# Kernel optimization log

Hardware: AMD Instinct MI355X
Metric: run time of the kernel (lower is better)

The kernel has to match this reference:

```python
import jax, jax.numpy as jnp
import numpy as np

ARCH = [128, 64, 32]
HIDDEN = 256
N_NODES = 20000
N_EDGES = 640000


def setup_inputs() -> dict:
    key = jax.random.key(0)
    ks = jax.random.split(key, 10)
    s = lambda fan_in: 1.0 / np.sqrt(fan_in)
    inp = {
        "x": jax.random.normal(ks[0], (N_NODES, ARCH[0]), dtype=jnp.float32),
        "edge_index": jax.random.randint(ks[1], (2, N_EDGES), 0, N_NODES, dtype=jnp.int64),
        # embedding: Linear(arch[0], hidden)
        "emb_W": jax.random.uniform(ks[2], (HIDDEN, ARCH[0]), jnp.float32, -s(ARCH[0]), s(ARCH[0])),
        "emb_b": jax.random.uniform(ks[3], (HIDDEN,), jnp.float32, -s(ARCH[0]), s(ARCH[0])),
        # message: Linear(hidden, hidden)
        "msg_W": jax.random.uniform(ks[4], (HIDDEN, HIDDEN), jnp.float32, -s(HIDDEN), s(HIDDEN)),
        "msg_b": jax.random.uniform(ks[5], (HIDDEN,), jnp.float32, -s(HIDDEN), s(HIDDEN)),
        # output_layers[0]: Linear(hidden, arch[0]*arch[1]) = 256 -> 8192
        "W0": jax.random.uniform(ks[6], (ARCH[0] * ARCH[1], HIDDEN), jnp.float32, -s(HIDDEN), s(HIDDEN)),
        "b0": jax.random.uniform(ks[7], (ARCH[0] * ARCH[1],), jnp.float32, -s(HIDDEN), s(HIDDEN)),
        # output_layers[1]: Linear(hidden, arch[1]*arch[2]) = 256 -> 2048
        "W1": jax.random.uniform(ks[8], (ARCH[1] * ARCH[2], HIDDEN), jnp.float32, -s(HIDDEN), s(HIDDEN)),
        "b1": jax.random.uniform(ks[9], (ARCH[1] * ARCH[2],), jnp.float32, -s(HIDDEN), s(HIDDEN)),
    }
    return inp


def reference(x, edge_index, emb_W, emb_b, msg_W, msg_b, W0, b0, W1, b1):
    # h = relu(embedding(x)): [N, hidden]
    h = jax.nn.relu(x @ emb_W.T + emb_b)
    row, col = edge_index[0], edge_index[1]
    # gather messages from source nodes, scatter-add into destinations
    agg = jnp.zeros_like(h).at[row].add(h[col])  # [N, hidden]
    h = jax.nn.relu(agg @ msg_W.T + msg_b)       # [N, hidden]
    # per-layer weight prediction: linear, reshape, mean over nodes
    w0 = (h @ W0.T + b0).mean(axis=0).reshape(ARCH[0], ARCH[1])  # [128, 64]
    w1 = (h @ W1.T + b1).mean(axis=0).reshape(ARCH[1], ARCH[2])  # [64, 32]
    return (w0, w1)
```

## Files before the change

### kernel.cpp

```cpp
#include <hip/hip_runtime.h>
#include <hip/hip_bf16.h>

#define N_NODES 20000
#define N_EDGES 640000
#define HID 256
#define INDIM 128

#define WS_H_OFF    0u
#define WS_AGG_OFF  5120000u
#define WS_EW_OFF   15360000u
#define WS_MW_OFF   15425536u
#define WS_CS_OFF   15556608u
#define WS_DEG_OFF  15557632u
#define WS_ROW_OFF  15637632u
#define WS_SRC_OFF  15717760u
#define WS_NEEDED   18277760u

#define EW_ELEMS (HID * INDIM)
#define MW_ELEMS (HID * HID)
#define CONV_BLOCKS ((EW_ELEMS + MW_ELEMS) / 8 / 256)
#define ZERO_BYTES  (1024 + 80000)
#define ZERO_F4     (ZERO_BYTES / 16)
#define ZERO_BLOCKS ((ZERO_F4 + 255) / 256)

#define EMB_BLOCKS  ((N_NODES + 63) / 64)
#define CNT_BLOCKS  (N_EDGES / 256)

typedef __attribute__((ext_vector_type(8))) short bf16x8;
typedef __attribute__((ext_vector_type(4))) float f32x4;
typedef __attribute__((ext_vector_type(2))) float f32x2;

__device__ inline unsigned short f2bf(float v) {
    union { float f; unsigned int u; } c; c.f = v;
    unsigned int lsb = (c.u >> 16) & 1u;
    c.u += 0x7fffu + lsb;
    return (unsigned short)(c.u >> 16);
}

__device__ inline unsigned char f2fp8(float v) {
    union { float f; unsigned int u; } c; c.f = v;
    if (v == 0.f) return 0;
    int e = (int)((c.u >> 23) & 0xff) - 127;
    if (e >= -6) {
        unsigned int mant = c.u & 0x7fffffu;
        unsigned int base = ((unsigned int)(e + 7) << 3) | (mant >> 20);
        unsigned int rem  = mant & 0xfffffu;
        base += (rem > 0x80000u) || (rem == 0x80000u && (base & 1u));
        return (unsigned char)base;
    } else {
        return (unsigned char)__builtin_rintf(v * 512.0f);
    }
}

__global__ __launch_bounds__(256) void k_convert(const float* __restrict__ eW,
                                                 const float* __restrict__ mW,
                                                 unsigned short* __restrict__ eWbf,
                                                 unsigned short* __restrict__ mWbf,
                                                 float4* __restrict__ zbase)
{
    if (blockIdx.x >= CONV_BLOCKS) {
        const int zi = (blockIdx.x - CONV_BLOCKS) * 256 + threadIdx.x;
        if (zi < ZERO_F4) zbase[zi] = make_float4(0.f, 0.f, 0.f, 0.f);
        return;
    }
    const int t = blockIdx.x * 256 + threadIdx.x;
    const int i8 = t * 8;
    const float* src;
    unsigned short* dst;
    int off;
    if (i8 < EW_ELEMS) { src = eW; dst = eWbf; off = i8; }
    else               { src = mW; dst = mWbf; off = i8 - EW_ELEMS; }

    float4 a = *(const float4*)(src + off);
    float4 b = *(const float4*)(src + off + 4);
    unsigned short o[8] = { f2bf(a.x), f2bf(a.y), f2bf(a.z), f2bf(a.w),
                            f2bf(b.x), f2bf(b.y), f2bf(b.z), f2bf(b.w) };
    *(bf16x8*)(dst + off) = *(bf16x8*)o;
}

__global__ __launch_bounds__(256) void k_embed_count(const float* __restrict__ x,
                                                     const unsigned short* __restrict__ Wbf,
                                                     const float* __restrict__ b,
                                                     unsigned char* __restrict__ h8,
                                                     const int* __restrict__ ei,
                                                     int* __restrict__ deg)
{
    if (blockIdx.x >= EMB_BLOCKS) {
        const int e = (blockIdx.x - EMB_BLOCKS) * 256 + threadIdx.x;
        if (e < N_EDGES) atomicAdd(&deg[ei[e]], 1);
        return;
    }

    const int tid  = threadIdx.x;
    const int wave = tid >> 6;
    const int lane = tid & 63;
    const int lr   = lane & 15;
    const int lq   = lane >> 4;
    const int n0   = blockIdx.x * 64;
    const int colbase = wave * 64;

    f32x4 acc[4][4] = {};

#pragma unroll
    for (int kk = 0; kk < INDIM; kk += 32) {
        bf16x8 a[4], bb[4];
#pragma unroll
        for (int g = 0; g < 4; ++g) {
            const float* xr = x + (size_t)(n0 + g * 16 + lr) * INDIM + kk + lq * 8;
            uint4 p0 = *(const uint4*)xr;
            uint4 p1 = *(const uint4*)(xr + 4);
            union { unsigned u[4]; bf16x8 v; } pk;
            pk.u[0] = ((p0.x + 0x8000u) >> 16) | ((p0.y + 0x8000u) & 0xFFFF0000u);
            pk.u[1] = ((p0.z + 0x8000u) >> 16) | ((p0.w + 0x8000u) & 0xFFFF0000u);
            pk.u[2] = ((p1.x + 0x8000u) >> 16) | ((p1.y + 0x8000u) & 0xFFFF0000u);
            pk.u[3] = ((p1.z + 0x8000u) >> 16) | ((p1.w + 0x8000u) & 0xFFFF0000u);
            a[g] = pk.v;
        }
#pragma unroll
        for (int c = 0; c < 4; ++c)
            bb[c] = *(const bf16x8*)(Wbf + (size_t)(colbase + c * 16 + lr) * INDIM + kk + lq * 8);
#pragma unroll
        for (int g = 0; g < 4; ++g)
#pragma unroll
            for (int c = 0; c < 4; ++c)
                acc[g][c] = __builtin_amdgcn_mfma_f32_16x16x32_bf16(a[g], bb[c], acc[g][c], 0, 0, 0);
    }

#pragma unroll
    for (int c = 0; c < 4; ++c) {
        const int j = colbase + c * 16 + lr;
        const float bias = b[j];
#pragma unroll
        for (int g = 0; g < 4; ++g) {
            const int nbase = n0 + g * 16 + lq * 4;
#pragma unroll
            for (int r = 0; r < 4; ++r) {
                const int n = nbase + r;
                if (n < N_NODES) {
                    float v = acc[g][c][r] + bias;
                    v = v > 0.f ? v : 0.f;
                    h8[(size_t)n * HID + j] = f2fp8(v);
                }
            }
        }
    }
}

__global__ __launch_bounds__(1024) void k_scan(const int* __restrict__ deg,
                                               int* __restrict__ rowstart)
{
    __shared__ int sums[1024];
    const int t = threadIdx.x;
    const int per = 20;
    const int base = t * per;

    int local[per];
    int s = 0;
#pragma unroll
    for (int i = 0; i < per; ++i) {
        int idx = base + i;
        int v = (idx < N_NODES) ? deg[idx] : 0;
        local[i] = s;
        s += v;
    }
    sums[t] = s;
    __syncthreads();

    for (int off = 1; off < 1024; off <<= 1) {
        int v = 0;
        if (t >= off) v = sums[t - off];
        __syncthreads();
        if (t >= off) sums[t] += v;
        __syncthreads();
    }

    const int pre = (t == 0) ? 0 : sums[t - 1];
#pragma unroll
    for (int i = 0; i < per; ++i) {
        int idx = base + i;
        if (idx < N_NODES) rowstart[idx] = pre + local[i];
    }
    if (t == 1023) rowstart[N_NODES] = sums[1023];
}

__global__ __launch_bounds__(256) void k_fill(const int* __restrict__ ei,
                                              const int* __restrict__ rowstart,
                                              int* __restrict__ deg,
                                              int* __restrict__ srcs)
{
    const int e = blockIdx.x * 256 + threadIdx.x;
    if (e >= N_EDGES) return;
    const int dst = ei[e];
    const int src = ei[N_EDGES + e];
    const int pos = rowstart[dst] + atomicSub(&deg[dst], 1) - 1;
    srcs[pos] = src;
}

__global__ __launch_bounds__(256) void k_gather(const int* __restrict__ rowstart,
                                                const int* __restrict__ srcs,
                                                const unsigned char* __restrict__ h8,
                                                unsigned short* __restrict__ aggbf)
{
    const int wid  = (blockIdx.x * 256 + threadIdx.x) >> 6;
    const int lane = threadIdx.x & 63;
    if (wid >= N_NODES) return;

    const int s0 = rowstart[wid];
    const int s1 = rowstart[wid + 1];
    const int qslot = lane >> 4;
    const int coff  = lane & 15;

    float4 acc[4] = { {0,0,0,0}, {0,0,0,0}, {0,0,0,0}, {0,0,0,0} };

#define DEC(V)                                                            \
    {   f32x2 t_;                                                         \
        t_ = __builtin_amdgcn_cvt_pk_f32_fp8((V).x, false);               \
        acc[0].x += t_[0]; acc[0].y += t_[1];                             \
        t_ = __builtin_amdgcn_cvt_pk_f32_fp8((V).x, true);                \
        acc[0].z += t_[0]; acc[0].w += t_[1];                             \
        t_ = __builtin_amdgcn_cvt_pk_f32_fp8((V).y, false);               \
        acc[1].x += t_[0]; acc[1].y += t_[1];                             \
        t_ = __builtin_amdgcn_cvt_pk_f32_fp8((V).y, true);                \
        acc[1].z += t_[0]; acc[1].w += t_[1];                             \
        t_ = __builtin_amdgcn_cvt_pk_f32_fp8((V).z, false);               \
        acc[2].x += t_[0]; acc[2].y += t_[1];                             \
        t_ = __builtin_amdgcn_cvt_pk_f32_fp8((V).z, true);                \
        acc[2].z += t_[0]; acc[2].w += t_[1];                             \
        t_ = __builtin_amdgcn_cvt_pk_f32_fp8((V).w, false);               \
        acc[3].x += t_[0]; acc[3].y += t_[1];                             \
        t_ = __builtin_amdgcn_cvt_pk_f32_fp8((V).w, true);                \
        acc[3].z += t_[0]; acc[3].w += t_[1];  }

    for (int base = s0; base < s1; base += 64) {
        const int rem = s1 - base;
        const int cnt = rem < 64 ? rem : 64;
        const int idx = (lane < rem) ? srcs[base + lane] : 0;
        int k = 0;
        for (; k + 8 <= cnt; k += 8) {
            const int sA = __shfl(idx, k + qslot);
            const int sB = __shfl(idx, k + 4 + qslot);
            uint4 vA = *((const uint4*)(h8 + (size_t)sA * 256) + coff);
            uint4 vB = *((const uint4*)(h8 + (size_t)sB * 256) + coff);
            DEC(vA);
            DEC(vB);
        }
        for (; k < cnt; k += 4) {
            const int sA = __shfl(idx, k + qslot);
            uint4 v = *((const uint4*)(h8 + (size_t)sA * 256) + coff);
            if (k + qslot >= cnt) { v.x = 0; v.y = 0; v.z = 0; v.w = 0; }
            DEC(v);
        }
    }
#undef DEC

#pragma unroll
    for (int j = 0; j < 4; ++j) {
        acc[j].x += __shfl_xor(acc[j].x, 16);
        acc[j].y += __shfl_xor(acc[j].y, 16);
        acc[j].z += __shfl_xor(acc[j].z, 16);
        acc[j].w += __shfl_xor(acc[j].w, 16);
        acc[j].x += __shfl_xor(acc[j].x, 32);
        acc[j].y += __shfl_xor(acc[j].y, 32);
        acc[j].z += __shfl_xor(acc[j].z, 32);
        acc[j].w += __shfl_xor(acc[j].w, 32);
    }

    if (qslot == 0) {
        unsigned short o[16];
#pragma unroll
        for (int j = 0; j < 4; ++j) {
            o[j * 4 + 0] = f2bf(acc[j].x);
            o[j * 4 + 1] = f2bf(acc[j].y);
            o[j * 4 + 2] = f2bf(acc[j].z);
            o[j * 4 + 3] = f2bf(acc[j].w);
        }
        unsigned short* dst = aggbf + (size_t)wid * HID + coff * 16;
        *(bf16x8*)dst       = *(bf16x8*)o;
        *(bf16x8*)(dst + 8) = *(bf16x8*)(o + 8);
    }
}

__global__ __launch_bounds__(256) void k_msg_mfma(const unsigned short* __restrict__ aggbf,
                                                  const unsigned short* __restrict__ Wbf,
                                                  const float* __restrict__ b,
                                                  float* __restrict__ colsum)
{
    const int tid  = threadIdx.x;
    const int wave = tid >> 6;
    const int lane = tid & 63;
    const int lr   = lane & 15;
    const int lq   = lane >> 4;
    const int n0   = blockIdx.x * 64;
    const int colbase = wave * 64;

    f32x4 acc[4][4] = {};

#pragma unroll
    for (int kk = 0; kk < HID; kk += 32) {
        bf16x8 a[4], bb[4];
#pragma unroll
        for (int g = 0; g < 4; ++g)
            a[g] = *(const bf16x8*)(aggbf + (size_t)(n0 + g * 16 + lr) * HID + kk + lq * 8);
#pragma unroll
        for (int c = 0; c < 4; ++c)
            bb[c] = *(const bf16x8*)(Wbf + (size_t)(colbase + c * 16 + lr) * HID + kk + lq * 8);
#pragma unroll
        for (int g = 0; g < 4; ++g)
#pragma unroll
            for (int c = 0; c < 4; ++c)
                acc[g][c] = __builtin_amdgcn_mfma_f32_16x16x32_bf16(a[g], bb[c], acc[g][c], 0, 0, 0);
    }

#pragma unroll
    for (int c = 0; c < 4; ++c) {
        const int j = colbase + c * 16 + lr;
        const float bias = b[j];
        float part = 0.f;
#pragma unroll
        for (int g = 0; g < 4; ++g) {
            if (n0 + g * 16 < N_NODES) {
#pragma unroll
                for (int r = 0; r < 4; ++r) {
                    float v = acc[g][c][r] + bias;
                    part += v > 0.f ? v : 0.f;
                }
            }
        }
        part += __shfl_xor(part, 16);
        part += __shfl_xor(part, 32);
        if (lane < 16) unsafeAtomicAdd(&colsum[j], part);
    }
}

__global__ __launch_bounds__(256) void k_out(const float* __restrict__ colsum,
                                             const float* __restrict__ W0,
                                             const float* __restrict__ b0,
                                             const float* __restrict__ W1,
                                             const float* __restrict__ b1,
                                             float* __restrict__ out)
{
    __shared__ float hm[HID];
    const int tid = threadIdx.x;
    hm[tid] = colsum[tid] * (1.0f / (float)N_NODES);
    __syncthreads();

    const int o = blockIdx.x * 256 + tid;
    const float* Wr;
    float bias;
    if (o < 8192) { Wr = W0 + (size_t)o * HID; bias = b0[o]; }
    else          { int o1 = o - 8192; Wr = W1 + (size_t)o1 * HID; bias = b1[o1]; }

    float s = bias;
    const float4* w4 = (const float4*)Wr;
    const float4* h4 = (const float4*)hm;
#pragma unroll 8
    for (int q = 0; q < 64; ++q) {
        float4 wv = w4[q];
        float4 hv = h4[q];
        s += wv.x * hv.x + wv.y * hv.y + wv.z * hv.z + wv.w * hv.w;
    }
    out[o] = s;
}

extern "C" void kernel_launch(void* const* d_in, const int* in_sizes, int n_in,
                              void* d_out, int out_size, void* d_ws, size_t ws_size,
                              hipStream_t stream)
{
    const float* x     = (const float*)d_in[0];
    const int*   ei    = (const int*)d_in[1];
    const float* emb_W = (const float*)d_in[2];
    const float* emb_b = (const float*)d_in[3];
    const float* msg_W = (const float*)d_in[4];
    const float* msg_b = (const float*)d_in[5];
    const float* W0    = (const float*)d_in[6];
    const float* b0    = (const float*)d_in[7];
    const float* W1    = (const float*)d_in[8];
    const float* b1    = (const float*)d_in[9];
    float* out = (float*)d_out;

    char* ws = (char*)d_ws;
    unsigned char*  h8    = (unsigned char*)(ws + WS_H_OFF);
    unsigned short* aggbf = (unsigned short*)(ws + WS_AGG_OFF);
    unsigned short* eWbf  = (unsigned short*)(ws + WS_EW_OFF);
    unsigned short* mWbf  = (unsigned short*)(ws + WS_MW_OFF);
    float* colsum = (float*)(ws + WS_CS_OFF);
    int* deg      = (int*)(ws + WS_DEG_OFF);
    int* rowstart = (int*)(ws + WS_ROW_OFF);
    int* srcs     = (int*)(ws + WS_SRC_OFF);

    k_convert<<<CONV_BLOCKS + ZERO_BLOCKS, 256, 0, stream>>>(
        emb_W, msg_W, eWbf, mWbf, (float4*)(ws + WS_CS_OFF));

    k_embed_count<<<EMB_BLOCKS + CNT_BLOCKS, 256, 0, stream>>>(
        x, eWbf, emb_b, h8, ei, deg);

    k_scan<<<1, 1024, 0, stream>>>(deg, rowstart);
    k_fill<<<CNT_BLOCKS, 256, 0, stream>>>(ei, rowstart, deg, srcs);

    k_gather<<<(N_NODES * 64 + 255) / 256, 256, 0, stream>>>(rowstart, srcs, h8, aggbf);

    k_msg_mfma<<<EMB_BLOCKS, 256, 0, stream>>>(aggbf, mWbf, msg_b, colsum);

    k_out<<<(8192 + 2048) / 256, 256, 0, stream>>>(colsum, W0, b0, W1, b1, out);
}
```

Measured before the change: 139.6 us.

## Halve node tile in embed and message GEMMs; use wave-shuffle scan

The embedding and message MFMA kernels now handle 32 nodes per block instead of 64. That doubles the block count (625 blocks) for better CU occupancy and removes the tail bounds checks, since 20000 divides by 32 evenly. The degree prefix scan replaces its 10-step shared-memory Hillis-Steele loop, which needed many __syncthreads, with warp-level __shfl_up scans plus a small per-wave sum array. The smaller tiles reload the weight fragments more often, which adds weight traffic in exchange for the extra parallelism.

```diff
diff --git a/kernel.cpp b/kernel.cpp
--- a/kernel.cpp
+++ b/kernel.cpp
@@ -23,7 +23,7 @@
 #define ZERO_F4     (ZERO_BYTES / 16)
 #define ZERO_BLOCKS ((ZERO_F4 + 255) / 256)
 
-#define EMB_BLOCKS  ((N_NODES + 63) / 64)
+#define EMB_BLOCKS  (N_NODES / 32)
 #define CNT_BLOCKS  (N_EDGES / 256)
 
 typedef __attribute__((ext_vector_type(8))) short bf16x8;
@@ -96,16 +96,16 @@
     const int lane = tid & 63;
     const int lr   = lane & 15;
     const int lq   = lane >> 4;
-    const int n0   = blockIdx.x * 64;
+    const int n0   = blockIdx.x * 32;
     const int colbase = wave * 64;
 
-    f32x4 acc[4][4] = {};
+    f32x4 acc[2][4] = {};
 
 #pragma unroll
     for (int kk = 0; kk < INDIM; kk += 32) {
-        bf16x8 a[4], bb[4];
-#pragma unroll
-        for (int g = 0; g < 4; ++g) {
+        bf16x8 a[2], bb[4];
+#pragma unroll
+        for (int g = 0; g < 2; ++g) {
             const float* xr = x + (size_t)(n0 + g * 16 + lr) * INDIM + kk + lq * 8;
             uint4 p0 = *(const uint4*)xr;
             uint4 p1 = *(const uint4*)(xr + 4);
@@ -120,7 +120,7 @@
         for (int c = 0; c < 4; ++c)
             bb[c] = *(const bf16x8*)(Wbf + (size_t)(colbase + c * 16 + lr) * INDIM + kk + lq * 8);
 #pragma unroll
-        for (int g = 0; g < 4; ++g)
+        for (int g = 0; g < 2; ++g)
 #pragma unroll
             for (int c = 0; c < 4; ++c)
                 acc[g][c] = __builtin_amdgcn_mfma_f32_16x16x32_bf16(a[g], bb[c], acc[g][c], 0, 0, 0);
@@ -131,16 +131,14 @@
         const int j = colbase + c * 16 + lr;
         const float bias = b[j];
 #pragma unroll
-        for (int g = 0; g < 4; ++g) {
+        for (int g = 0; g < 2; ++g) {
             const int nbase = n0 + g * 16 + lq * 4;
 #pragma unroll
             for (int r = 0; r < 4; ++r) {
                 const int n = nbase + r;
-                if (n < N_NODES) {
-                    float v = acc[g][c][r] + bias;
-                    v = v > 0.f ? v : 0.f;
-                    h8[(size_t)n * HID + j] = f2fp8(v);
-                }
+                float v = acc[g][c][r] + bias;
+                v = v > 0.f ? v : 0.f;
+                h8[(size_t)n * HID + j] = f2fp8(v);
             }
         }
     }
@@ -149,38 +147,50 @@
 __global__ __launch_bounds__(1024) void k_scan(const int* __restrict__ deg,
                                                int* __restrict__ rowstart)
 {
-    __shared__ int sums[1024];
-    const int t = threadIdx.x;
-    const int per = 20;
-    const int base = t * per;
-
-    int local[per];
+    __shared__ int wsum[16];
+    const int t  = threadIdx.x;
+    const int wv = t >> 6;
+    const int ln = t & 63;
+    const int base = t * 20;
+
+    int local[20];
     int s = 0;
 #pragma unroll
-    for (int i = 0; i < per; ++i) {
+    for (int i = 0; i < 20; ++i) {
         int idx = base + i;
         int v = (idx < N_NODES) ? deg[idx] : 0;
         local[i] = s;
         s += v;
     }
-    sums[t] = s;
+
+    int inc = s;
+#pragma unroll
+    for (int d = 1; d < 64; d <<= 1) {
+        int u = __shfl_up(inc, d);
+        if (ln >= d) inc += u;
+    }
+    if (ln == 63) wsum[wv] = inc;
     __syncthreads();
 
-    for (int off = 1; off < 1024; off <<= 1) {
-        int v = 0;
-        if (t >= off) v = sums[t - off];
-        __syncthreads();
-        if (t >= off) sums[t] += v;
-        __syncthreads();
-    }
-
-    const int pre = (t == 0) ? 0 : sums[t - 1];
-#pragma unroll
-    for (int i = 0; i < per; ++i) {
+    if (wv == 0) {
+        int v = (ln < 16) ? wsum[ln] : 0;
+        int i2 = v;
+#pragma unroll
+        for (int d = 1; d < 16; d <<= 1) {
+            int u = __shfl_up(i2, d);
+            if (ln >= d) i2 += u;
+        }
+        if (ln < 16) wsum[ln] = i2 - v;
+    }
+    __syncthreads();
+
+    const int pre = wsum[wv] + inc - s;
+#pragma unroll
+    for (int i = 0; i < 20; ++i) {
         int idx = base + i;
         if (idx < N_NODES) rowstart[idx] = pre + local[i];
     }
-    if (t == 1023) rowstart[N_NODES] = sums[1023];
+    if (t == 1023) rowstart[N_NODES] = pre + s;
 }
 
 __global__ __launch_bounds__(256) void k_fill(const int* __restrict__ ei,
@@ -290,22 +300,22 @@
     const int lane = tid & 63;
     const int lr   = lane & 15;
     const int lq   = lane >> 4;
-    const int n0   = blockIdx.x * 64;
+    const int n0   = blockIdx.x * 32;
     const int colbase = wave * 64;
 
-    f32x4 acc[4][4] = {};
+    f32x4 acc[2][4] = {};
 
 #pragma unroll
     for (int kk = 0; kk < HID; kk += 32) {
-        bf16x8 a[4], bb[4];
-#pragma unroll
-        for (int g = 0; g < 4; ++g)
+        bf16x8 a[2], bb[4];
+#pragma unroll
+        for (int g = 0; g < 2; ++g)
             a[g] = *(const bf16x8*)(aggbf + (size_t)(n0 + g * 16 + lr) * HID + kk + lq * 8);
 #pragma unroll
         for (int c = 0; c < 4; ++c)
             bb[c] = *(const bf16x8*)(Wbf + (size_t)(colbase + c * 16 + lr) * HID + kk + lq * 8);
 #pragma unroll
-        for (int g = 0; g < 4; ++g)
+        for (int g = 0; g < 2; ++g)
 #pragma unroll
             for (int c = 0; c < 4; ++c)
                 acc[g][c] = __builtin_amdgcn_mfma_f32_16x16x32_bf16(a[g], bb[c], acc[g][c], 0, 0, 0);
@@ -317,13 +327,11 @@
         const float bias = b[j];
         float part = 0.f;
 #pragma unroll
-        for (int g = 0; g < 4; ++g) {
-            if (n0 + g * 16 < N_NODES) {
-#pragma unroll
-                for (int r = 0; r < 4; ++r) {
-                    float v = acc[g][c][r] + bias;
-                    part += v > 0.f ? v : 0.f;
-                }
+        for (int g = 0; g < 2; ++g) {
+#pragma unroll
+            for (int r = 0; r < 4; ++r) {
+                float v = acc[g][c][r] + bias;
+                part += v > 0.f ? v : 0.f;
             }
         }
         part += __shfl_xor(part, 16);
```

After: 151.9 us. 8.8% more time.
